# Optimization experiments

Measured on AMD Instinct MI355X. Metric: run time of the kernel, lower is better.

## Reference

```python
import jax, jax.numpy as jnp
import numpy as np

L = 248      # max_clip_seq_len
WIN = 3      # window_size
H = 8        # attention heads
D = 768      # input/output dim
HID = 256    # rope hidden dim
SIGMA = 2.0
EPS_LN = 1e-5


def _layernorm(x, g, b):
    m = jnp.mean(x, axis=-1, keepdims=True)
    v = jnp.var(x, axis=-1, keepdims=True)
    return (x - m) / jnp.sqrt(v + EPS_LN) * g + b


def _normalize(x):
    n = jnp.linalg.norm(x, axis=-1, keepdims=True)
    return x / jnp.maximum(n, 1e-12)


def _peb_forward(word_feat, text_feat_full, word_pos, ctx_W, ctx_b, in_W, in_b,
                 out_W, out_b, cn_g, cn_b, r1_W, r1_b, ln_g, ln_b, r2_W, r2_b,
                 pos_emb, pos_temp):
    B, N, _ = word_feat.shape
    valid = word_pos != -1                              # [B,N] bool
    vf = valid.astype(word_feat.dtype)[..., None]       # [B,N,1]
    wp = jnp.clip(word_pos, 0, L - 1)                   # [B,N]
    half = WIN // 2
    offs = jnp.arange(-half, half + 1)
    positions = jnp.clip(wp[..., None] + offs[None, None, :], 0, L - 1)
    ctx = text_feat_full[jnp.arange(B)[:, None, None], positions]
    ctx_anchor = (ctx.reshape(B, N, WIN * D) @ ctx_W + ctx_b) * vf       # [B,N,D]
    q = word_feat * vf                                  # word_proj is Identity (768->768)
    # MultiheadAttention (batch_first), query=q, key=value=ctx_anchor
    hd = D // H
    qp = (q @ in_W[:, :D] + in_b[:D]).reshape(B, N, H, hd)
    kp = (ctx_anchor @ in_W[:, D:2 * D] + in_b[D:2 * D]).reshape(B, N, H, hd)
    vp = (ctx_anchor @ in_W[:, 2 * D:] + in_b[2 * D:]).reshape(B, N, H, hd)
    scores = jnp.einsum('bqhd,bkhd->bhqk', qp, kp) / jnp.sqrt(jnp.asarray(hd, q.dtype))
    attn = jax.nn.softmax(scores, axis=-1)
    ao = jnp.einsum('bhqk,bkhd->bqhd', attn, vp).reshape(B, N, D)
    attn_out = ao @ out_W + out_b
    x = _layernorm(q + attn_out, cn_g, cn_b) * vf       # word_feat_with_ctx
    # rope_mapping: Linear -> GELU -> LayerNorm -> Linear
    rope = _layernorm(jax.nn.gelu(x @ r1_W + r1_b, approximate=False), ln_g, ln_b) @ r2_W + r2_b
    rope_n = _normalize(rope)
    clip_ref_n = _normalize(pos_emb)                    # [L,D]
    temp = jnp.maximum(pos_temp, 0.001)
    logits = jnp.einsum('bnd,ld->bnl', rope_n, clip_ref_n) / temp
    log_q = jax.nn.log_softmax(logits, axis=-1)
    # gaussian soft target over L positions
    pos_idx = jnp.arange(L, dtype=jnp.float32)
    d2 = (pos_idx[None, None, :] - wp[..., None].astype(jnp.float32)) ** 2
    targ = jnp.exp(-d2 / (2.0 * SIGMA ** 2))
    targ = targ / (targ.sum(axis=-1, keepdims=True) + 1e-12)
    lqv = log_q * vf
    tv = targ * vf
    n_valid = valid.sum().astype(jnp.float32)
    safe_t = jnp.where(tv > 0, tv, 1.0)
    kl = jnp.sum(jnp.where(tv > 0, tv * (jnp.log(safe_t) - lqv), 0.0)) / (n_valid + 1e-12)
    # relative position loss on cosine similarity
    pos_sim01 = (jnp.einsum('bnd,bmd->bnm', rope_n, rope_n) + 1.0) / 2.0
    wpf = wp.astype(jnp.float32)
    target_sim = 1.0 - jnp.abs(wpf[:, :, None] - wpf[:, None, :]) / float(L)
    vm2 = vf[:, :, 0][:, None, :] * vf[:, :, 0][:, :, None]
    rel = jnp.sum((pos_sim01 * vm2 - target_sim * vm2) ** 2) / (vm2.sum() + 1e-12)
    peb_loss = (1.0 * kl + 0.5 * rel) * 1.0             # kl_weight=1, rel_weight=0.5, peb_weight=1
    # scatter blended positional features to 248-length sequence (vectorized over batch)
    vals = 0.8 * pos_emb[wp] + 0.2 * rope               # [B,N,D]
    pos_s = jnp.where(valid, wp, L)                     # invalid -> OOB index, dropped
    emb = jnp.zeros((B, L, D), word_feat.dtype).at[jnp.arange(B)[:, None], pos_s].set(vals, mode='drop')
    return emb, peb_loss, kl, rel


def setup_inputs() -> dict:
    key = jax.random.key(0)
    ks = jax.random.split(key, 20)
    B, N = 128, 128
    word_feat = jax.random.normal(ks[0], (B, N, D), jnp.float32)
    text_feat_full = jax.random.normal(ks[1], (B, L, D), jnp.float32)
    # unique sorted positions per batch (scatter is then deterministic, matching torch)
    perms = jax.vmap(lambda k: jax.random.permutation(k, L))(jax.random.split(ks[2], B))
    word_pos = jnp.sort(perms[:, :N], axis=-1).astype(jnp.int32)
    s = 0.02
    return {
        'word_feat': word_feat,
        'text_feat_full': text_feat_full,
        'word_pos': word_pos,
        'ctx_W': s * jax.random.normal(ks[3], (WIN * D, D), jnp.float32),
        'ctx_b': s * jax.random.normal(ks[4], (D,), jnp.float32),
        'in_W': s * jax.random.normal(ks[5], (D, 3 * D), jnp.float32),
        'in_b': s * jax.random.normal(ks[6], (3 * D,), jnp.float32),
        'out_W': s * jax.random.normal(ks[7], (D, D), jnp.float32),
        'out_b': s * jax.random.normal(ks[8], (D,), jnp.float32),
        'cn_g': jnp.ones((D,), jnp.float32) + s * jax.random.normal(ks[9], (D,), jnp.float32),
        'cn_b': s * jax.random.normal(ks[10], (D,), jnp.float32),
        'r1_W': s * jax.random.normal(ks[11], (D, HID), jnp.float32),
        'r1_b': s * jax.random.normal(ks[12], (HID,), jnp.float32),
        'ln_g': jnp.ones((HID,), jnp.float32) + s * jax.random.normal(ks[13], (HID,), jnp.float32),
        'ln_b': s * jax.random.normal(ks[14], (HID,), jnp.float32),
        'r2_W': s * jax.random.normal(ks[15], (HID, D), jnp.float32),
        'r2_b': s * jax.random.normal(ks[16], (D,), jnp.float32),
        'pos_emb': jax.random.normal(ks[17], (L, D), jnp.float32),
        'pos_temp': jnp.asarray(1.0, jnp.float32),
    }


def reference(word_feat, text_feat_full, word_pos, ctx_W, ctx_b, in_W, in_b,
              out_W, out_b, cn_g, cn_b, r1_W, r1_b, ln_g, ln_b, r2_W, r2_b,
              pos_emb, pos_temp):
    return _peb_forward(word_feat, text_feat_full, word_pos, ctx_W, ctx_b, in_W, in_b,
                        out_W, out_b, cn_g, cn_b, r1_W, r1_b, ln_g, ln_b, r2_W, r2_b,
                        pos_emb, pos_temp)
```

## Files before the change

kernel.cpp:

```cpp
#include <hip/hip_runtime.h>
#include <math.h>

#define BB   128
#define NN   128
#define LL   248
#define DD   768
#define HH   8
#define HDh  96
#define HIDN 256
#define MROWS (BB*NN)
#define MB_   (1u<<20)
#define KVLD 1536

typedef unsigned short u16;
typedef unsigned int   u32;
typedef __attribute__((ext_vector_type(8))) short s16x8;
typedef __attribute__((ext_vector_type(4))) float f32x4;

__device__ __forceinline__ u16 f2bf(float x) {
    u32 u = __float_as_uint(x);
    u32 r = u + 0x7fffu + ((u >> 16) & 1u);
    return (u16)(r >> 16);
}
__device__ __forceinline__ float bf2f(u16 h) {
    return __uint_as_float(((u32)h) << 16);
}
__device__ __forceinline__ void gload16(const void* g, void* l) {
    __builtin_amdgcn_global_load_lds(
        (const __attribute__((address_space(1))) void*)g,
        (__attribute__((address_space(3))) void*)l, 16, 0, 0);
}

template<int NT>
__device__ __forceinline__ float breduce_sum(float v, float* red) {
    const int tid = threadIdx.x;
    red[tid] = v; __syncthreads();
#pragma unroll
    for (int o = NT / 2; o > 0; o >>= 1) {
        if (tid < o) red[tid] += red[tid + o];
        __syncthreads();
    }
    float r = red[0]; __syncthreads();
    return r;
}
__device__ __forceinline__ double breduce_sum_d256(double v, double* red) {
    const int tid = threadIdx.x;
    red[tid] = v; __syncthreads();
#pragma unroll
    for (int o = 128; o > 0; o >>= 1) {
        if (tid < o) red[tid] += red[tid + o];
        __syncthreads();
    }
    double r = red[0]; __syncthreads();
    return r;
}

#define TEXT_F4 (BB*LL*DD/4)
#define Q_F4    (MROWS*(DD/4))
__global__ __launch_bounds__(256)
void prep_all_kernel(const float* __restrict__ ctx_W, u16* __restrict__ ctx_Wt,
                     const float* __restrict__ in_W,  u16* __restrict__ in_Wt,
                     const float* __restrict__ out_W, u16* __restrict__ out_Wt,
                     const float* __restrict__ r1_W,  u16* __restrict__ r1_Wt,
                     const float* __restrict__ r2_W,  u16* __restrict__ r2_Wt,
                     const float* __restrict__ text,  u16* __restrict__ textb,
                     const float* __restrict__ wf,    u16* __restrict__ qb,
                     const int* __restrict__ wpos,    int* __restrict__ cpos,
                     const float* __restrict__ pe,    u16* __restrict__ clipb,
                     float* __restrict__ zbias) {
    __shared__ float smem[32 * 33];
    int bid = blockIdx.x;
    const int tid = threadIdx.x;

    if (bid < 4416) {
        const float* src; u16* dst; int C;
        if (bid < 1728)      { src = ctx_W; dst = ctx_Wt; C = 768;  }
        else if (bid < 3456) { src = in_W;  dst = in_Wt;  C = 2304; bid -= 1728; }
        else if (bid < 4032) { src = out_W; dst = out_Wt; C = 768;  bid -= 3456; }
        else if (bid < 4224) { src = r1_W;  dst = r1_Wt;  C = 256;  bid -= 4032; }
        else                 { src = r2_W;  dst = r2_Wt;  C = 768;  bid -= 4224; }
        const int R = (C == 768) ? ((dst == ctx_Wt) ? 2304 : ((dst == out_Wt) ? 768 : 256))
                                 : 768;
        const int ct = C >> 5;
        const int r0 = (bid / ct) * 32, c0 = (bid % ct) * 32;
        const int tx = tid & 31, ty = tid >> 5;
#pragma unroll
        for (int i = 0; i < 32; i += 8)
            smem[(ty + i) * 33 + tx] = src[(size_t)(r0 + ty + i) * C + c0 + tx];
        __syncthreads();
#pragma unroll
        for (int i = 0; i < 32; i += 8)
            dst[(size_t)(c0 + ty + i) * R + r0 + tx] = f2bf(smem[tx * 33 + ty + i]);
    } else if (bid < 4672) {
        const int l = bid - 4416;
        if (l >= LL) {
            for (int j = 0; j < 3; ++j) clipb[(size_t)l * DD + tid + j * 256] = 0;
            return;
        }
        float t[3]; float q = 0.f;
#pragma unroll
        for (int j = 0; j < 3; ++j) {
            t[j] = pe[(size_t)l * DD + tid + j * 256];
            q = fmaf(t[j], t[j], q);
        }
        q = breduce_sum<256>(q, smem);
        float inv = 1.f / fmaxf(sqrtf(q), 1e-12f);
#pragma unroll
        for (int j = 0; j < 3; ++j)
            clipb[(size_t)l * DD + tid + j * 256] = f2bf(t[j] * inv);
    } else {
        const int ebid = bid - 4672;
        if (ebid == 0) {
            for (int r = tid; r < MROWS; r += 256) {
                int w = wpos[r];
                cpos[r] = w < 0 ? 0 : (w > LL - 1 ? LL - 1 : w);
            }
            if (tid < 256) zbias[tid] = 0.f;
        }
        const int lane = tid & 63;
        const int wid = ebid * 4 + (tid >> 6);
        const int NCHUNK = (TEXT_F4 + Q_F4) / 512;
        for (int c = wid; c < NCHUNK; c += 8192) {
            const int base = c * 512;
            if (base < TEXT_F4) {
                const float4* sp = (const float4*)text;
                uint2* op = (uint2*)textb;
                float4 v[8];
#pragma unroll
                for (int j = 0; j < 8; ++j)
                    v[j] = sp[(size_t)base + j * 64 + lane];
#pragma unroll
                for (int j = 0; j < 8; ++j) {
                    uint2 o;
                    o.x = (u32)f2bf(v[j].x) | ((u32)f2bf(v[j].y) << 16);
                    o.y = (u32)f2bf(v[j].z) | ((u32)f2bf(v[j].w) << 16);
                    op[(size_t)base + j * 64 + lane] = o;
                }
            } else {
                const int qb4 = base - TEXT_F4;
                const float4* sp = (const float4*)wf;
                uint2* op = (uint2*)qb;
                float4 v[8]; float vfm[8];
#pragma unroll
                for (int j = 0; j < 8; ++j)
                    v[j] = sp[(size_t)qb4 + j * 64 + lane];
#pragma unroll
                for (int j = 0; j < 8; ++j)
                    vfm[j] = (wpos[(qb4 + j * 64 + lane) / 192] != -1) ? 1.f : 0.f;
#pragma unroll
                for (int j = 0; j < 8; ++j) {
                    uint2 o;
                    o.x = (u32)f2bf(v[j].x * vfm[j]) | ((u32)f2bf(v[j].y * vfm[j]) << 16);
                    o.y = (u32)f2bf(v[j].z * vfm[j]) | ((u32)f2bf(v[j].w * vfm[j]) << 16);
                    op[(size_t)qb4 + j * 64 + lane] = o;
                }
            }
        }
    }
}

template<int GATHER, int CBF16, int MASK>
__device__ __forceinline__ void gemm_tile(
    const int m0, const int n0,
    const u16* __restrict__ A,
    const u16* __restrict__ TXT,
    const int* __restrict__ cpos,
    const u16* __restrict__ Bt,
    const float* __restrict__ bias,
    void* __restrict__ Cout, int ldc, int K,
    const int* __restrict__ wpos,
    u16* Alds, u16* Blds) {
    const int tid = threadIdx.x;
    const int l = tid & 63, wv = tid >> 6;

    const int rw = wv * 8 + (l >> 3);
    const int ce = ((l & 7) ^ (l >> 3)) << 3;
    u16* Ad0 = Alds + wv * 512;
    u16* Bd0 = Blds + wv * 512;

    const int wm = (wv >> 1) * 64, wn = (wv & 1) * 64;
    const int la = l & 15, lg = l >> 4;

    int aoff[4], boff[4];
#pragma unroll
    for (int m = 0; m < 4; ++m) {
        int ra = wm + m * 16 + la;
        aoff[m] = ra * 64 + (((lg ^ (la & 7)) << 3));
        int rb = wn + m * 16 + la;
        boff[m] = rb * 64 + (((lg ^ (la & 7)) << 3));
    }

    const u16* pb[4];
#pragma unroll
    for (int i = 0; i < 4; ++i)
        pb[i] = Bt + (size_t)(n0 + rw + i * 32) * K + ce;

    f32x4 acc[4][4] = {};

    auto do_step = [&](const u16* a0, const u16* a1, const u16* a2, const u16* a3,
                       const u16* b0, const u16* b1, const u16* b2, const u16* b3) {
        gload16(a0, Ad0);
        gload16(a1, Ad0 + 2048);
        gload16(a2, Ad0 + 4096);
        gload16(a3, Ad0 + 6144);
        gload16(b0, Bd0);
        gload16(b1, Bd0 + 2048);
        gload16(b2, Bd0 + 4096);
        gload16(b3, Bd0 + 6144);
        __syncthreads();
#pragma unroll
        for (int kk = 0; kk < 2; ++kk) {
            const int kx = kk << 5;
            s16x8 af[4], bf[4];
#pragma unroll
            for (int m = 0; m < 4; ++m) af[m] = *(const s16x8*)(Alds + (aoff[m] ^ kx));
#pragma unroll
            for (int n = 0; n < 4; ++n) bf[n] = *(const s16x8*)(Blds + (boff[n] ^ kx));
#pragma unroll
            for (int m = 0; m < 4; ++m)
#pragma unroll
                for (int n = 0; n < 4; ++n)
                    acc[m][n] = __builtin_amdgcn_mfma_f32_16x16x32_bf16(
                        af[m], bf[n], acc[m][n], 0, 0, 0);
        }
        __syncthreads();
    };

    if constexpr (GATHER) {
        int gb[4], gc[4];
#pragma unroll
        for (int i = 0; i < 4; ++i) {
            int g = m0 + rw + i * 32;
            gb[i] = g >> 7;
            gc[i] = cpos[g];
        }
#pragma unroll 1
        for (int w = 0; w < 3; ++w) {
            const u16* pa[4];
#pragma unroll
            for (int i = 0; i < 4; ++i) {
                int p = gc[i] + w - 1;
                p = p < 0 ? 0 : (p > LL - 1 ? LL - 1 : p);
                pa[i] = TXT + ((size_t)(gb[i] * LL + p)) * DD + ce;
            }
            const u16* b0 = pb[0] + w * DD; const u16* b1 = pb[1] + w * DD;
            const u16* b2 = pb[2] + w * DD; const u16* b3 = pb[3] + w * DD;
#pragma unroll 1
            for (int kt = 0; kt < 12; ++kt)
                do_step(pa[0] + kt * 64, pa[1] + kt * 64, pa[2] + kt * 64, pa[3] + kt * 64,
                        b0 + kt * 64, b1 + kt * 64, b2 + kt * 64, b3 + kt * 64);
        }
    } else {
        const u16* pa[4];
#pragma unroll
        for (int i = 0; i < 4; ++i)
            pa[i] = A + (size_t)(m0 + rw + i * 32) * K + ce;
        const int nk = K >> 6;
#pragma unroll 1
        for (int kt = 0; kt < nk; ++kt)
            do_step(pa[0] + (kt << 6), pa[1] + (kt << 6), pa[2] + (kt << 6), pa[3] + (kt << 6),
                    pb[0] + (kt << 6), pb[1] + (kt << 6), pb[2] + (kt << 6), pb[3] + (kt << 6));
    }

#pragma unroll
    for (int m = 0; m < 4; ++m) {
        const int rb = m0 + wm + m * 16 + lg * 4;
        float vf[4];
        if constexpr (MASK) {
#pragma unroll
            for (int r = 0; r < 4; ++r) vf[r] = (wpos[rb + r] != -1) ? 1.f : 0.f;
        }
#pragma unroll
        for (int n = 0; n < 4; ++n) {
            const int col = n0 + wn + n * 16 + la;
            const float bv = bias[col];
#pragma unroll
            for (int r = 0; r < 4; ++r) {
                float o = acc[m][n][r] + bv;
                if constexpr (MASK) o *= vf[r];
                if constexpr (CBF16)
                    ((u16*)Cout)[(size_t)(rb + r) * ldc + col] = f2bf(o);
                else
                    ((float*)Cout)[(size_t)(rb + r) * ldc + col] = o;
            }
        }
    }
}

template<int GATHER, int CBF16, int MASK>
__global__ __launch_bounds__(256)
void gemm_bt(const u16* __restrict__ A,
             const u16* __restrict__ TXT,
             const int* __restrict__ cpos,
             const u16* __restrict__ Bt,
             const float* __restrict__ bias,
             void* __restrict__ Cout, int ldc, int K,
             const int* __restrict__ wpos) {
    __shared__ __align__(16) u16 Alds[128 * 64];
    __shared__ __align__(16) u16 Blds[128 * 64];
    const int gx  = gridDim.x;
    const int hw  = blockIdx.y * gx + blockIdx.x;
    const int nwg = gx * gridDim.y;
    const int cpx = nwg >> 3;
    const int lin = (hw & 7) * cpx + (hw >> 3);
    const int m0 = (lin / gx) * 128, n0 = (lin % gx) * 128;
    gemm_tile<GATHER, CBF16, MASK>(m0, n0, A, TXT, cpos, Bt, bias,
                                   Cout, ldc, K, wpos, Alds, Blds);
}

__global__ __launch_bounds__(256)
void gemm_ctx_qp_kernel(const u16* __restrict__ textb, const int* __restrict__ cpos,
                        const u16* __restrict__ ctx_Wt, const float* __restrict__ ctx_b,
                        u16* __restrict__ ctxa,
                        const u16* __restrict__ qb, const u16* __restrict__ in_Wt,
                        const float* __restrict__ in_b, u16* __restrict__ qpb,
                        const int* __restrict__ wpos) {
    __shared__ __align__(16) u16 Alds[128 * 64];
    __shared__ __align__(16) u16 Blds[128 * 64];
    const int bid = blockIdx.x;
    if (bid < 768) {
        const int lin = (bid & 7) * 96 + (bid >> 3);
        const int m0 = (lin / 6) * 128, n0 = (lin % 6) * 128;
        gemm_tile<1, 1, 1>(m0, n0, nullptr, textb, cpos, ctx_Wt, ctx_b,
                           ctxa, DD, 3 * DD, wpos, Alds, Blds);
    } else {
        const int b2 = bid - 768;
        const int lin = (b2 & 7) * 96 + (b2 >> 3);
        const int m0 = (lin / 6) * 128, n0 = (lin % 6) * 128;
        gemm_tile<0, 1, 0>(m0, n0, qb, nullptr, nullptr, in_Wt, in_b,
                           qpb, DD, DD, nullptr, Alds, Blds);
    }
}

__device__ __forceinline__ void rel_tile(int blk, const u16* __restrict__ rnb,
                                         const int* __restrict__ wpos,
                                         float* __restrict__ rel_part,
                                         float* __restrict__ vm2_part,
                                         u16* T ) {
    float* red = (float*)(T + 4096);
    const int b = blk >> 1, jh = blk & 1;
    const int tid = threadIdx.x;
    const int l = tid & 63, wv = tid >> 6;
    const int la = l & 15, lg = l >> 4;

    const int f0 = wv * 1024 + l * 16;
    const int f1 = f0 + 4096;
    const int rA0 = f0 >> 6, rA1 = f1 >> 6;
    const int ce0 = ((f0 & 63) ^ (((rA0 >> 1) & 3) << 4)) >> 1;
    const int ce1 = ((f1 & 63) ^ (((rA1 >> 1) & 3) << 4)) >> 1;
    const u16* src0 = rnb + ((size_t)(b * NN + rA0)) * DD + ce0;
    const u16* src1 = rnb + ((size_t)(b * NN + rA1)) * DD + ce1;
    u16* dst0 = T + wv * 512;
    u16* dst1 = T + 2048 + wv * 512;

    int aoff[2];
#pragma unroll
    for (int g = 0; g < 2; ++g) {
        int ra = wv * 32 + g * 16 + la;
        aoff[g] = ra * 32 + ((lg * 8) ^ (((ra >> 1) & 3) << 3));
    }
    int boff[4];
#pragma unroll
    for (int nf = 0; nf < 4; ++nf) {
        int rb = jh * 64 + nf * 16 + la;
        boff[nf] = rb * 32 + ((lg * 8) ^ (((rb >> 1) & 3) << 3));
    }

    f32x4 acc[2][4] = {};
    for (int kt = 0; kt < 24; ++kt) {
        gload16(src0 + kt * 32, dst0);
        gload16(src1 + kt * 32, dst1);
        __syncthreads();
        s16x8 a[2], bf_[4];
#pragma unroll
        for (int g = 0; g < 2; ++g) a[g] = *(const s16x8*)(T + aoff[g]);
#pragma unroll
        for (int nf = 0; nf < 4; ++nf) bf_[nf] = *(const s16x8*)(T + boff[nf]);
#pragma unroll
        for (int g = 0; g < 2; ++g)
#pragma unroll
            for (int nf = 0; nf < 4; ++nf)
                acc[g][nf] = __builtin_amdgcn_mfma_f32_16x16x32_bf16(
                    a[g], bf_[nf], acc[g][nf], 0, 0, 0);
        __syncthreads();
    }

    float csum = 0.f, msum = 0.f;
#pragma unroll
    for (int g = 0; g < 2; ++g) {
        float wif[4], vi[4];
#pragma unroll
        for (int r = 0; r < 4; ++r) {
            int wi = wpos[b * NN + wv * 32 + g * 16 + lg * 4 + r];
            vi[r] = (wi != -1) ? 1.f : 0.f;
            wif[r] = (float)(wi < 0 ? 0 : (wi > LL - 1 ? LL - 1 : wi));
        }
#pragma unroll
        for (int nf = 0; nf < 4; ++nf) {
            int wj = wpos[b * NN + jh * 64 + nf * 16 + la];
            float vj = (wj != -1) ? 1.f : 0.f;
            float wjf = (float)(wj < 0 ? 0 : (wj > LL - 1 ? LL - 1 : wj));
#pragma unroll
            for (int r = 0; r < 4; ++r) {
                float sim = (acc[g][nf][r] + 1.f) * 0.5f;
                float ts  = 1.f - fabsf(wif[r] - wjf) * (1.f / (float)LL);
                float m2  = vi[r] * vj;
                float df  = m2 * (sim - ts);
                csum += df * df;
                msum += m2;
            }
        }
    }
    csum = breduce_sum<256>(csum, red);
    msum = breduce_sum<256>(msum, red);
    if (tid == 0) { rel_part[blk] = csum; vm2_part[blk] = msum; }
}

__global__ __launch_bounds__(256)
void logits_rel_kernel(const u16* __restrict__ rnb, const u16* __restrict__ clipb,
                       const float* __restrict__ zbias, float* __restrict__ logits,
                       const int* __restrict__ wpos,
                       float* __restrict__ relp, float* __restrict__ vmp) {
    __shared__ __align__(16) u16 pool[2 * 128 * 64];
    const int bid = blockIdx.x;
    if (bid < 256) {
        const int lin = (bid & 7) * 32 + (bid >> 3);
        const int m0 = (lin >> 1) * 128, n0 = (lin & 1) * 128;
        gemm_tile<0, 0, 0>(m0, n0, rnb, nullptr, nullptr, clipb, zbias,
                           logits, 256, DD, nullptr, pool, pool + 128 * 64);
    } else {
        rel_tile(bid - 256, rnb, wpos, relp, vmp, pool);
    }
}

__global__ __launch_bounds__(512)
void attn_mfma_kernel(const u16* __restrict__ qp, const u16* __restrict__ kvb,
                      u16* __restrict__ ao) {
    __shared__ __align__(16) u16 K_lds[128 * 96];
    __shared__ __align__(16) u16 Vt_lds[96 * 128];
    __shared__ __align__(16) u16 P_lds[128 * 128];
    const int bh = blockIdx.x;
    const int b = bh >> 3, h = bh & 7;
    const int tid = threadIdx.x;
    const int l = tid & 63, wv = tid >> 6;
    const int la = l & 15, lg = l >> 4;
    const float scale = 0.10206207261596575f;

    const size_t qbase  = ((size_t)b * NN) * DD + h * HDh;
    const size_t kvbase = ((size_t)b * NN) * KVLD + h * HDh;

#pragma unroll
    for (int i = 0; i < 3; ++i) {
        int f = i * 8192 + wv * 1024 + l * 16;
        int row = f / 192;
        int inner = f - row * 192;
        gload16((const char*)(kvb + kvbase + (size_t)row * KVLD) + inner,
                (char*)K_lds + f);
    }

    uint4 vchunk[3]; int vkey[3], vd0[3];
#pragma unroll
    for (int i = 0; i < 3; ++i) {
        int c = tid + i * 512;
        int key = c / 12, dc = c - key * 12;
        vkey[i] = key; vd0[i] = dc * 8;
        vchunk[i] = *(const uint4*)(kvb + kvbase + (size_t)key * KVLD + DD + dc * 8);
    }

    const int q0 = wv * 16;
    s16x8 qf[3];
#pragma unroll
    for (int kt = 0; kt < 3; ++kt)
        qf[kt] = *(const s16x8*)(qp + qbase + (size_t)(q0 + la) * DD + kt * 32 + lg * 8);

#pragma unroll
    for (int i = 0; i < 3; ++i) {
        const u16* e = (const u16*)&vchunk[i];
#pragma unroll
        for (int j = 0; j < 8; ++j) {
            int d = vd0[i] + j;
            int byte = ((d * 128 + vkey[i]) * 2) ^ ((d & 7) << 4);
            *(u16*)((char*)Vt_lds + byte) = e[j];
        }
    }
    __syncthreads();

    f32x4 sacc[8] = {};
#pragma unroll
    for (int kt = 0; kt < 3; ++kt) {
#pragma unroll
        for (int nf = 0; nf < 8; ++nf) {
            s16x8 bfr = *(const s16x8*)(K_lds + (nf * 16 + la) * 96 + kt * 32 + lg * 8);
            sacc[nf] = __builtin_amdgcn_mfma_f32_16x16x32_bf16(qf[kt], bfr, sacc[nf], 0, 0, 0);
        }
    }

#pragma unroll
    for (int r = 0; r < 4; ++r) {
        float m = -1e30f;
#pragma unroll
        for (int nf = 0; nf < 8; ++nf) m = fmaxf(m, sacc[nf][r]);
#pragma unroll
        for (int o = 8; o > 0; o >>= 1) m = fmaxf(m, __shfl_xor(m, o, 64));
        m *= scale;
        float p[8]; float s = 0.f;
#pragma unroll
        for (int nf = 0; nf < 8; ++nf) { p[nf] = expf(sacc[nf][r] * scale - m); s += p[nf]; }
#pragma unroll
        for (int o = 8; o > 0; o >>= 1) s += __shfl_xor(s, o, 64);
        const float inv = 1.f / s;
        const int q = q0 + lg * 4 + r;
#pragma unroll
        for (int nf = 0; nf < 8; ++nf) {
            int byte = ((q * 128 + nf * 16 + la) * 2) ^ ((q & 7) << 4);
            *(u16*)((char*)P_lds + byte) = f2bf(p[nf] * inv);
        }
    }
    __syncthreads();

    f32x4 oacc[6] = {};
#pragma unroll
    for (int kk = 0; kk < 4; ++kk) {
        const int qrow = q0 + la;
        int abyte = ((qrow * 128 + kk * 32 + lg * 8) * 2) ^ ((qrow & 7) << 4);
        s16x8 af = *(const s16x8*)((char*)P_lds + abyte);
#pragma unroll
        for (int nf = 0; nf < 6; ++nf) {
            const int d = nf * 16 + la;
            int bbyte = ((d * 128 + kk * 32 + lg * 8) * 2) ^ ((d & 7) << 4);
            s16x8 bfr = *(const s16x8*)((char*)Vt_lds + bbyte);
            oacc[nf] = __builtin_amdgcn_mfma_f32_16x16x32_bf16(af, bfr, oacc[nf], 0, 0, 0);
        }
    }

#pragma unroll
    for (int nf = 0; nf < 6; ++nf) {
#pragma unroll
        for (int r = 0; r < 4; ++r) {
            const int q = q0 + lg * 4 + r;
            ao[qbase + (size_t)q * DD + nf * 16 + la] = f2bf(oacc[nf][r]);
        }
    }
}

__global__ __launch_bounds__(256)
void ln768_kernel(const u16* __restrict__ qb, const u16* __restrict__ at,
                  const int* __restrict__ wpos, const float* __restrict__ g,
                  const float* __restrict__ bta, u16* __restrict__ xout) {
    __shared__ float red[256];
    const int r = blockIdx.x, tid = threadIdx.x;
    const float vf = (wpos[r] != -1) ? 1.f : 0.f;
    float t[3]; float s = 0.f, q = 0.f;
#pragma unroll
    for (int j = 0; j < 3; ++j) {
        int d = tid + j * 256;
        t[j] = bf2f(qb[(size_t)r * DD + d]) + bf2f(at[(size_t)r * DD + d]);
        s += t[j];
        q = fmaf(t[j], t[j], q);
    }
    s = breduce_sum<256>(s, red);
    q = breduce_sum<256>(q, red);
    float mean = s * (1.f / DD);
    float var  = q * (1.f / DD) - mean * mean;
    float inv  = 1.f / sqrtf(var + 1e-5f);
#pragma unroll
    for (int j = 0; j < 3; ++j) {
        int d = tid + j * 256;
        xout[(size_t)r * DD + d] = f2bf(((t[j] - mean) * inv * g[d] + bta[d]) * vf);
    }
}

__global__ __launch_bounds__(256)
void ln256_gelu_kernel(const u16* __restrict__ g1, const float* __restrict__ lg,
                       const float* __restrict__ lb, u16* __restrict__ hout) {
    __shared__ float red[256];
    const int r = blockIdx.x, tid = threadIdx.x;
    float v  = bf2f(g1[(size_t)r * HIDN + tid]);
    float ge = 0.5f * v * (1.f + erff(v * 0.7071067811865475f));
    float s = breduce_sum<256>(ge, red);
    float q = breduce_sum<256>(ge * ge, red);
    float mean = s * (1.f / HIDN);
    float var  = q * (1.f / HIDN) - mean * mean;
    float inv  = 1.f / sqrtf(var + 1e-5f);
    hout[(size_t)r * HIDN + tid] = f2bf((ge - mean) * inv * lg[tid] + lb[tid]);
}

__global__ __launch_bounds__(256)
void norm_emb_kernel(const u16* __restrict__ ropeb, const float* __restrict__ pe,
                     const int* __restrict__ wpos, u16* __restrict__ rnb,
                     float* __restrict__ emb) {
    __shared__ float red[256];
    const int bid = blockIdx.x;
    const int tid = threadIdx.x;
    if (bid < MROWS) {
        const int r = bid;
        float t[3]; float q = 0.f;
#pragma unroll
        for (int j = 0; j < 3; ++j) {
            t[j] = bf2f(ropeb[(size_t)r * DD + tid + j * 256]);
            q = fmaf(t[j], t[j], q);
        }
        q = breduce_sum<256>(q, red);
        float inv = 1.f / fmaxf(sqrtf(q), 1e-12f);
#pragma unroll
        for (int j = 0; j < 3; ++j)
            rnb[(size_t)r * DD + tid + j * 256] = f2bf(t[j] * inv);
    } else {
        const int bl = bid - MROWS;
        const int b = bl / LL, l = bl - b * LL;
        const int* wp = wpos + b * NN;
        int lo = 0, hi = NN - 1, found = -1;
        while (lo <= hi) {
            int mid = (lo + hi) >> 1;
            int v = wp[mid];
            if (v == l) { found = mid; break; }
            if (v < l) lo = mid + 1; else hi = mid - 1;
        }
        float* dst = emb + (size_t)bl * DD;
        if (found >= 0) {
            const u16* rr = ropeb + (size_t)(b * NN + found) * DD;
#pragma unroll
            for (int j = 0; j < 3; ++j) {
                int d = tid + j * 256;
                dst[d] = 0.8f * pe[(size_t)l * DD + d] + 0.2f * bf2f(rr[d]);
            }
        } else {
#pragma unroll
            for (int j = 0; j < 3; ++j)
                dst[tid + j * 256] = 0.f;
        }
    }
}

__global__ __launch_bounds__(256)
void kl_lite_kernel(const float* __restrict__ logits, const int* __restrict__ wpos,
                    const float* __restrict__ pos_temp, float* __restrict__ klp) {
    const int row = blockIdx.x * 4 + (threadIdx.x >> 6);
    const int l = threadIdx.x & 63;
    const float invt = 1.f / fmaxf(pos_temp[0], 0.001f);
    const float* lrow = logits + (size_t)row * 256;

    float lg[4];
#pragma unroll
    for (int q = 0; q < 4; ++q) {
        int c = l + q * 64;
        lg[q] = (c < LL) ? lrow[c] * invt : -1e30f;
    }
    float m = fmaxf(fmaxf(lg[0], lg[1]), fmaxf(lg[2], lg[3]));
#pragma unroll
    for (int o = 32; o > 0; o >>= 1) m = fmaxf(m, __shfl_xor(m, o, 64));

    float S = 0.f;
#pragma unroll
    for (int q = 0; q < 4; ++q) S += expf(lg[q] - m);
#pragma unroll
    for (int o = 32; o > 0; o >>= 1) S += __shfl_xor(S, o, 64);
    const float logZ = m + logf(S);

    const int wr = wpos[row];
    const bool valid = (wr != -1);
    const int wp = wr < 0 ? 0 : (wr > LL - 1 ? LL - 1 : wr);

    float targ[4]; float tsum = 0.f;
#pragma unroll
    for (int q = 0; q < 4; ++q) {
        int c = l + q * 64;
        float dl = (float)c - (float)wp;
        targ[q] = (c < LL) ? expf(-dl * dl * 0.125f) : 0.f;
        tsum += targ[q];
    }
#pragma unroll
    for (int o = 32; o > 0; o >>= 1) tsum += __shfl_xor(tsum, o, 64);
    const float tden = 1.f / (tsum + 1e-12f);

    float c_ = 0.f;
#pragma unroll
    for (int q = 0; q < 4; ++q) {
        float tn = targ[q] * tden;
        if (valid && tn > 0.f) c_ += tn * (logf(tn) - (lg[q] - logZ));
    }
#pragma unroll
    for (int o = 32; o > 0; o >>= 1) c_ += __shfl_xor(c_, o, 64);
    if (l == 0) klp[row] = c_;
}

__global__ __launch_bounds__(256)
void final_kernel(const float* __restrict__ klp, const float* __restrict__ relp,
                  const float* __restrict__ vmp, const int* __restrict__ wpos,
                  float* __restrict__ outs) {
    __shared__ double rd[256];
    const int tid = threadIdx.x;
    double kl = 0.0, rel = 0.0, vm = 0.0, nv = 0.0;
    for (int r = tid; r < MROWS; r += 256) {
        kl += (double)klp[r];
        nv += (wpos[r] != -1) ? 1.0 : 0.0;
    }
    if (tid < 256) {
        rel += (double)relp[tid];
        vm  += (double)vmp[tid];
    }
    kl  = breduce_sum_d256(kl, rd);
    rel = breduce_sum_d256(rel, rd);
    vm  = breduce_sum_d256(vm, rd);
    nv  = breduce_sum_d256(nv, rd);
    if (tid == 0) {
        float klf  = (float)(kl / (nv + 1e-12));
        float relf = (float)(rel / (vm + 1e-12));
        outs[0] = klf + 0.5f * relf;
        outs[1] = klf;
        outs[2] = relf;
    }
}

extern "C" void kernel_launch(void* const* d_in, const int* in_sizes, int n_in,
                              void* d_out, int out_size, void* d_ws, size_t ws_size,
                              hipStream_t stream) {
    (void)in_sizes; (void)n_in; (void)ws_size; (void)out_size;

    const float* word_feat = (const float*)d_in[0];
    const float* text      = (const float*)d_in[1];
    const int*   wpos      = (const int*)d_in[2];
    const float* ctx_W     = (const float*)d_in[3];
    const float* ctx_b     = (const float*)d_in[4];
    const float* in_W      = (const float*)d_in[5];
    const float* in_b      = (const float*)d_in[6];
    const float* out_W     = (const float*)d_in[7];
    const float* out_b     = (const float*)d_in[8];
    const float* cn_g      = (const float*)d_in[9];
    const float* cn_b      = (const float*)d_in[10];
    const float* r1_W      = (const float*)d_in[11];
    const float* r1_b      = (const float*)d_in[12];
    const float* ln_g      = (const float*)d_in[13];
    const float* ln_b      = (const float*)d_in[14];
    const float* r2_W      = (const float*)d_in[15];
    const float* r2_b      = (const float*)d_in[16];
    const float* pos_emb   = (const float*)d_in[17];
    const float* pos_temp  = (const float*)d_in[18];

    char* W = (char*)d_ws;
    u16*   ctx_Wt = (u16*)(W);
    u16*   in_Wt  = ctx_Wt + (size_t)768 * 2304;
    u16*   out_Wt = in_Wt  + (size_t)2304 * 768;
    u16*   r1_Wt  = out_Wt + (size_t)768 * 768;
    u16*   r2_Wt  = r1_Wt  + (size_t)256 * 768;
    u16*   clipb  = r2_Wt + (size_t)768 * 256;
    int*   cposb  = (int*)(clipb + (size_t)256 * DD);
    float* klp    = (float*)(cposb + MROWS);
    float* relp   = klp + MROWS;
    float* vmp    = relp + 256;
    float* zbias  = vmp + 256;
    u16*   textb  = (u16*)(W + (size_t)12 * MB_);
    u16*   atoutb = textb;
    float* logits = (float*)(W + (size_t)12 * MB_);
    u16*   xb     = (u16*)(W + (size_t)36 * MB_);
    u16*   qb     = (u16*)(W + (size_t)60 * MB_);
    u16*   ctxa   = (u16*)(W + (size_t)86 * MB_);
    u16*   aob    = ctxa;
    u16*   rnb    = ctxa;
    u16*   qpb    = (u16*)(W + (size_t)112 * MB_);
    u16*   g1b    = (u16*)(W + (size_t)112 * MB_);
    u16*   hb     = (u16*)(W + (size_t)128 * MB_);
    u16*   kvb    = (u16*)(W + (size_t)138 * MB_);
    u16*   ropeb  = kvb;

    dim3 blk(256);

    prep_all_kernel<<<dim3(4416 + 256 + 2048), blk, 0, stream>>>(
        ctx_W, ctx_Wt, in_W, in_Wt, out_W, out_Wt, r1_W, r1_Wt, r2_W, r2_Wt,
        text, textb, word_feat, qb, wpos, cposb, pos_emb, clipb, zbias);

    dim3 g768(6, 128);
    dim3 g1536(12, 128);

    gemm_ctx_qp_kernel<<<dim3(1536), blk, 0, stream>>>(
        textb, cposb, ctx_Wt, ctx_b, ctxa, qb, in_Wt, in_b, qpb, wpos);
    gemm_bt<0, 1, 0><<<g1536, blk, 0, stream>>>(
        ctxa, nullptr, nullptr, in_Wt + (size_t)768 * 768, in_b + DD, kvb, KVLD, DD, nullptr);
    attn_mfma_kernel<<<dim3(BB * HH), dim3(512), 0, stream>>>(qpb, kvb, aob);
    gemm_bt<0, 1, 0><<<g768, blk, 0, stream>>>(
        aob, nullptr, nullptr, out_Wt, out_b, atoutb, DD, DD, nullptr);
    ln768_kernel<<<dim3(MROWS), blk, 0, stream>>>(qb, atoutb, wpos, cn_g, cn_b, xb);
    gemm_bt<0, 1, 0><<<dim3(2, 128), blk, 0, stream>>>(
        xb, nullptr, nullptr, r1_Wt, r1_b, g1b, HIDN, DD, nullptr);
    ln256_gelu_kernel<<<dim3(MROWS), blk, 0, stream>>>(g1b, ln_g, ln_b, hb);
    gemm_bt<0, 1, 0><<<g768, blk, 0, stream>>>(
        hb, nullptr, nullptr, r2_Wt, r2_b, ropeb, DD, HIDN, nullptr);
    norm_emb_kernel<<<dim3(MROWS + BB * LL), blk, 0, stream>>>(
        ropeb, pos_emb, wpos, rnb, (float*)d_out);
    logits_rel_kernel<<<dim3(512), blk, 0, stream>>>(
        rnb, clipb, zbias, logits, wpos, relp, vmp);
    kl_lite_kernel<<<dim3(MROWS / 4), blk, 0, stream>>>(logits, wpos, pos_temp, klp);
    final_kernel<<<dim3(1), blk, 0, stream>>>(
        klp, relp, vmp, wpos, (float*)d_out + (size_t)BB * LL * DD);
}
```

Measured before the change: 433.1 us.

## Double-buffer LDS tiles in shared GEMM tile to overlap loads with MFMA

Restructures the shared gemm_tile K loop to use two LDS buffers. The next k-tile's global-to-LDS loads are issued before the MFMA work on the current tile, leaving one barrier per step instead of two. The gather path is flattened into a single 36-step loop with precomputed per-window row pointers. LDS per block doubles to 64 KB, which may reduce occupancy. The rel_tile path also shares the enlarged pool.

```diff
diff --git a/kernel.cpp b/kernel.cpp
--- a/kernel.cpp
+++ b/kernel.cpp
@@ -175,8 +175,6 @@
 
     const int rw = wv * 8 + (l >> 3);
     const int ce = ((l & 7) ^ (l >> 3)) << 3;
-    u16* Ad0 = Alds + wv * 512;
-    u16* Bd0 = Blds + wv * 512;
 
     const int wm = (wv >> 1) * 64, wn = (wv & 1) * 64;
     const int la = l & 15, lg = l >> 4;
@@ -195,27 +193,65 @@
     for (int i = 0; i < 4; ++i)
         pb[i] = Bt + (size_t)(n0 + rw + i * 32) * K + ce;
 
+    const u16* pa[4];
+    const u16* paw0[4]; const u16* paw1[4]; const u16* paw2[4];
+    if constexpr (GATHER) {
+#pragma unroll
+        for (int i = 0; i < 4; ++i) {
+            int g = m0 + rw + i * 32;
+            int gb = g >> 7, gc = cpos[g];
+            int p0 = gc - 1; p0 = p0 < 0 ? 0 : p0;
+            int p1 = gc;
+            int p2 = gc + 1; p2 = p2 > LL - 1 ? LL - 1 : p2;
+            paw0[i] = TXT + ((size_t)(gb * LL + p0)) * DD + ce;
+            paw1[i] = TXT + ((size_t)(gb * LL + p1)) * DD + ce;
+            paw2[i] = TXT + ((size_t)(gb * LL + p2)) * DD + ce;
+        }
+    } else {
+#pragma unroll
+        for (int i = 0; i < 4; ++i)
+            pa[i] = A + (size_t)(m0 + rw + i * 32) * K + ce;
+    }
+
+    auto STAGE = [&](int buf, int kt) {
+        u16* Ad = Alds + buf * 8192 + wv * 512;
+        u16* Bd = Blds + buf * 8192 + wv * 512;
+        if constexpr (GATHER) {
+            const int w = (kt >= 24) ? 2 : ((kt >= 12) ? 1 : 0);
+            const int kin = kt - w * 12;
+#pragma unroll
+            for (int i = 0; i < 4; ++i) {
+                const u16* ai = (w == 0) ? paw0[i] : ((w == 1) ? paw1[i] : paw2[i]);
+                gload16(ai + kin * 64, Ad + i * 2048);
+            }
+        } else {
+#pragma unroll
+            for (int i = 0; i < 4; ++i)
+                gload16(pa[i] + kt * 64, Ad + i * 2048);
+        }
+#pragma unroll
+        for (int i = 0; i < 4; ++i)
+            gload16(pb[i] + kt * 64, Bd + i * 2048);
+    };
+
     f32x4 acc[4][4] = {};
-
-    auto do_step = [&](const u16* a0, const u16* a1, const u16* a2, const u16* a3,
-                       const u16* b0, const u16* b1, const u16* b2, const u16* b3) {
-        gload16(a0, Ad0);
-        gload16(a1, Ad0 + 2048);
-        gload16(a2, Ad0 + 4096);
-        gload16(a3, Ad0 + 6144);
-        gload16(b0, Bd0);
-        gload16(b1, Bd0 + 2048);
-        gload16(b2, Bd0 + 4096);
-        gload16(b3, Bd0 + 6144);
-        __syncthreads();
+    const int nk = GATHER ? 36 : (K >> 6);
+
+    STAGE(0, 0);
+    __syncthreads();
+#pragma unroll 1
+    for (int kt = 0; kt < nk; ++kt) {
+        const int cur = kt & 1;
+        if (kt + 1 < nk) STAGE(cur ^ 1, kt + 1);
+        const int cb = cur * 8192;
 #pragma unroll
         for (int kk = 0; kk < 2; ++kk) {
             const int kx = kk << 5;
             s16x8 af[4], bf[4];
 #pragma unroll
-            for (int m = 0; m < 4; ++m) af[m] = *(const s16x8*)(Alds + (aoff[m] ^ kx));
-#pragma unroll
-            for (int n = 0; n < 4; ++n) bf[n] = *(const s16x8*)(Blds + (boff[n] ^ kx));
+            for (int m = 0; m < 4; ++m) af[m] = *(const s16x8*)(Alds + cb + (aoff[m] ^ kx));
+#pragma unroll
+            for (int n = 0; n < 4; ++n) bf[n] = *(const s16x8*)(Blds + cb + (boff[n] ^ kx));
 #pragma unroll
             for (int m = 0; m < 4; ++m)
 #pragma unroll
@@ -224,42 +260,6 @@
                         af[m], bf[n], acc[m][n], 0, 0, 0);
         }
         __syncthreads();
-    };
-
-    if constexpr (GATHER) {
-        int gb[4], gc[4];
-#pragma unroll
-        for (int i = 0; i < 4; ++i) {
-            int g = m0 + rw + i * 32;
-            gb[i] = g >> 7;
-            gc[i] = cpos[g];
-        }
-#pragma unroll 1
-        for (int w = 0; w < 3; ++w) {
-            const u16* pa[4];
-#pragma unroll
-            for (int i = 0; i < 4; ++i) {
-                int p = gc[i] + w - 1;
-                p = p < 0 ? 0 : (p > LL - 1 ? LL - 1 : p);
-                pa[i] = TXT + ((size_t)(gb[i] * LL + p)) * DD + ce;
-            }
-            const u16* b0 = pb[0] + w * DD; const u16* b1 = pb[1] + w * DD;
-            const u16* b2 = pb[2] + w * DD; const u16* b3 = pb[3] + w * DD;
-#pragma unroll 1
-            for (int kt = 0; kt < 12; ++kt)
-                do_step(pa[0] + kt * 64, pa[1] + kt * 64, pa[2] + kt * 64, pa[3] + kt * 64,
-                        b0 + kt * 64, b1 + kt * 64, b2 + kt * 64, b3 + kt * 64);
-        }
-    } else {
-        const u16* pa[4];
-#pragma unroll
-        for (int i = 0; i < 4; ++i)
-            pa[i] = A + (size_t)(m0 + rw + i * 32) * K + ce;
-        const int nk = K >> 6;
-#pragma unroll 1
-        for (int kt = 0; kt < nk; ++kt)
-            do_step(pa[0] + (kt << 6), pa[1] + (kt << 6), pa[2] + (kt << 6), pa[3] + (kt << 6),
-                    pb[0] + (kt << 6), pb[1] + (kt << 6), pb[2] + (kt << 6), pb[3] + (kt << 6));
     }
 
 #pragma unroll
@@ -296,8 +296,7 @@
              const float* __restrict__ bias,
              void* __restrict__ Cout, int ldc, int K,
              const int* __restrict__ wpos) {
-    __shared__ __align__(16) u16 Alds[128 * 64];
-    __shared__ __align__(16) u16 Blds[128 * 64];
+    __shared__ __align__(16) u16 AB[4 * 128 * 64];
     const int gx  = gridDim.x;
     const int hw  = blockIdx.y * gx + blockIdx.x;
     const int nwg = gx * gridDim.y;
@@ -305,7 +304,7 @@
     const int lin = (hw & 7) * cpx + (hw >> 3);
     const int m0 = (lin / gx) * 128, n0 = (lin % gx) * 128;
     gemm_tile<GATHER, CBF16, MASK>(m0, n0, A, TXT, cpos, Bt, bias,
-                                   Cout, ldc, K, wpos, Alds, Blds);
+                                   Cout, ldc, K, wpos, AB, AB + 2 * 8192);
 }
 
 __global__ __launch_bounds__(256)
@@ -315,20 +314,19 @@
                         const u16* __restrict__ qb, const u16* __restrict__ in_Wt,
                         const float* __restrict__ in_b, u16* __restrict__ qpb,
                         const int* __restrict__ wpos) {
-    __shared__ __align__(16) u16 Alds[128 * 64];
-    __shared__ __align__(16) u16 Blds[128 * 64];
+    __shared__ __align__(16) u16 AB[4 * 128 * 64];
     const int bid = blockIdx.x;
     if (bid < 768) {
         const int lin = (bid & 7) * 96 + (bid >> 3);
         const int m0 = (lin / 6) * 128, n0 = (lin % 6) * 128;
         gemm_tile<1, 1, 1>(m0, n0, nullptr, textb, cpos, ctx_Wt, ctx_b,
-                           ctxa, DD, 3 * DD, wpos, Alds, Blds);
+                           ctxa, DD, 3 * DD, wpos, AB, AB + 2 * 8192);
     } else {
         const int b2 = bid - 768;
         const int lin = (b2 & 7) * 96 + (b2 >> 3);
         const int m0 = (lin / 6) * 128, n0 = (lin % 6) * 128;
         gemm_tile<0, 1, 0>(m0, n0, qb, nullptr, nullptr, in_Wt, in_b,
-                           qpb, DD, DD, nullptr, Alds, Blds);
+                           qpb, DD, DD, nullptr, AB, AB + 2 * 8192);
     }
 }
 
@@ -421,13 +419,13 @@
                        const float* __restrict__ zbias, float* __restrict__ logits,
                        const int* __restrict__ wpos,
                        float* __restrict__ relp, float* __restrict__ vmp) {
-    __shared__ __align__(16) u16 pool[2 * 128 * 64];
+    __shared__ __align__(16) u16 pool[4 * 128 * 64];
     const int bid = blockIdx.x;
     if (bid < 256) {
         const int lin = (bid & 7) * 32 + (bid >> 3);
         const int m0 = (lin >> 1) * 128, n0 = (lin & 1) * 128;
         gemm_tile<0, 0, 0>(m0, n0, rnb, nullptr, nullptr, clipb, zbias,
-                           logits, 256, DD, nullptr, pool, pool + 128 * 64);
+                           logits, 256, DD, nullptr, pool, pool + 2 * 8192);
     } else {
         rel_tile(bid - 256, rnb, wpos, relp, vmp, pool);
     }
```

Measured after the change: 400.7 us. -7.5%, faster.
